# Optimization experiments

Hardware: AMD Instinct MI355X
Metric: run time of the kernel (lower is better)

Reference implementation:

```python
import jax, jax.numpy as jnp
import numpy as np
from jax import lax

B, S, D, H, HFF, T = 256, 33, 42, 128, 256, 20
BN_EPS = 1e-5

def _bn(x, g, b):
    # eval-mode BatchNorm1d with running_mean=0, running_var=1
    return x * (g / jnp.sqrt(1.0 + BN_EPS)) + b

def _gelu(x):
    return jax.nn.gelu(x, approximate=False)  # torch default GELU (exact)

def setup_inputs() -> dict:
    key = jax.random.key(0)
    ks = iter(jax.random.split(key, 48))
    w = lambda shp, s=0.02: jax.random.normal(next(ks), shp, dtype=jnp.float32) * s
    z = lambda shp: jnp.zeros(shp, jnp.float32)
    o = lambda shp: jnp.ones(shp, jnp.float32)
    inp = {
        'interaction_path': jax.random.normal(next(ks), (B, S, D), dtype=jnp.float32),
        'timestamps': jnp.broadcast_to(jnp.arange(S, dtype=jnp.float32) * 0.1, (B, S)),
        # initial encoder: Linear(42->128), BN, GELU, Linear(128->128), BN
        'enc_w1': w((D, H)), 'enc_b1': z(H), 'enc_g1': o(H), 'enc_be1': z(H),
        'enc_w2': w((H, H)), 'enc_b2': z(H), 'enc_g2': o(H), 'enc_be2': z(H),
        # vector field: 128->256 (BN,GELU), 256->256 (BN,GELU) x2, 256->5376
        'vf_w0': w((H, HFF)), 'vf_b0': z(HFF), 'vf_g0': o(HFF), 'vf_be0': z(HFF),
        'vf_w1': w((HFF, HFF)), 'vf_b1': z(HFF), 'vf_g1': o(HFF), 'vf_be1': z(HFF),
        'vf_w2': w((HFF, HFF)), 'vf_b2': z(HFF), 'vf_g2': o(HFF), 'vf_be2': z(HFF),
        'vf_w3': w((HFF, H * D)), 'vf_b3': z(H * D),
        # multihead attention (seq_len = 1 -> softmax is identically 1)
        'wv': w((H, H)), 'bv': z(H), 'wo': w((H, H)), 'bo': z(H),
        # 20 trait decoders, stacked: 128->64->32->1
        'dw1': w((T, H, 64)), 'db1': z((T, 64)),
        'dw2': w((T, 64, 32)), 'db2': z((T, 32)),
        'dw3': w((T, 32, 1)), 'db3': z((T, 1)),
    }
    return inp

def reference(interaction_path, timestamps,
              enc_w1, enc_b1, enc_g1, enc_be1, enc_w2, enc_b2, enc_g2, enc_be2,
              vf_w0, vf_b0, vf_g0, vf_be0, vf_w1, vf_b1, vf_g1, vf_be1,
              vf_w2, vf_b2, vf_g2, vf_be2, vf_w3, vf_b3,
              wv, bv, wo, bo,
              dw1, db1, dw2, db2, dw3, db3):
    b = interaction_path.shape[0]
    # ---- initial encoder on X[:, 0] ----
    x0 = interaction_path[:, 0]                      # [B, D]
    h = _gelu(_bn(x0 @ enc_w1 + enc_b1, enc_g1, enc_be1))
    z0 = _bn(h @ enc_w2 + enc_b2, enc_g2, enc_be2)   # [B, H]

    # ---- CDE vector field: z -> [B, H, D] ----
    def vf(zz):
        y = _gelu(_bn(zz @ vf_w0 + vf_b0, vf_g0, vf_be0))
        y = _gelu(_bn(y @ vf_w1 + vf_b1, vf_g1, vf_be1))
        y = _gelu(_bn(y @ vf_w2 + vf_b2, vf_g2, vf_be2))
        return (y @ vf_w3 + vf_b3).reshape(b, H, D)

    def g(zz, dxdt):  # f(z) @ dX/dt  -> [B, H]
        return jnp.einsum('bhd,bd->bh', vf(zz), dxdt)

    # linear-interpolation control path: piecewise-constant derivative
    t = timestamps[0]                                # [S]
    dt = t[1:] - t[:-1]                              # [S-1]
    dX = interaction_path[:, 1:] - interaction_path[:, :-1]   # [B, S-1, D]
    dXdt = dX / dt[None, :, None]                    # [B, S-1, D]

    def step(zz, x):
        dxdt, hstep = x
        k1 = g(zz, dxdt)
        k2 = g(zz + 0.5 * hstep * k1, dxdt)
        k3 = g(zz + 0.5 * hstep * k2, dxdt)
        k4 = g(zz + hstep * k3, dxdt)
        return zz + (hstep / 6.0) * (k1 + 2.0 * k2 + 2.0 * k3 + k4), None

    zT, _ = lax.scan(step, z0, (jnp.swapaxes(dXdt, 0, 1), dt))  # [B, H]

    # ---- self-attention over a length-1 sequence: softmax==1 -> out_proj(v) ----
    attended = (zT @ wv + bv) @ wo + bo              # [B, H]

    # ---- 20 trait decoders (stacked / vectorized) ----
    h1 = _gelu(jnp.einsum('bh,thd->tbd', attended, dw1) + db1[:, None, :])
    h2 = _gelu(jnp.einsum('tbd,tde->tbe', h1, dw2) + db2[:, None, :])
    out = jax.nn.sigmoid(jnp.einsum('tbe,teo->tbo', h2, dw3) + db3[:, None, :])
    return jnp.transpose(out[..., 0], (1, 0))        # [B, 20]
```

## Files before the change

### kernel.cpp

```cpp
#include <hip/hip_runtime.h>
#include <cstdint>

constexpr int B    = 256;
constexpr int S    = 33;
constexpr int D    = 42;
constexpr int H    = 128;
constexpr int HFF  = 256;
constexpr int T    = 20;
constexpr int NSTEP = S - 1;
constexpr int DP   = D / 2;
constexpr int ADW  = 8192;
constexpr int CH   = 16;
#define BN_SCALE 0.9999950000374997f

typedef _Float16 h2v __attribute__((ext_vector_type(2)));
union UH2 { uint32_t u; h2v h; };

__device__ __forceinline__ float fdot2u(uint32_t a, uint32_t b, float c) {
    UH2 x, y; x.u = a; y.u = b;
    return __builtin_amdgcn_fdot2(x.h, y.h, c, false);
}
__device__ __forceinline__ uint32_t packh2(float a, float b) {
    UH2 u; u.h = h2v{(_Float16)a, (_Float16)b}; return u.u;
}
__device__ __forceinline__ float gelu_exact(float x) {
    return 0.5f * x * (1.0f + erff(x * 0.70710678118654752f));
}
__device__ __forceinline__ float gelu_fast(float x) {
    float inner = x * (1.0f + 0.044715f * x * x);
    float E = __expf(1.5957691216f * inner);
    return x * E * __frcp_rn(E + 1.0f);
}

__global__ void pack_kernel(const float* __restrict__ w0, const float* __restrict__ w1,
                            const float* __restrict__ w2, const float* __restrict__ w3,
                            uint32_t* __restrict__ wcol, uint32_t* __restrict__ wq) {
    int idx = blockIdx.x * 256 + threadIdx.x;
    if (idx < 160 * 512) {
        int r = idx >> 9, t = idx & 511;
        int j = t >> 1, half = t & 1;
        float a, bb;
        if (r < 32)      { int ip = half * 32 + r;      a = w0[(2*ip)*HFF + j]; bb = w0[(2*ip+1)*HFF + j]; }
        else if (r < 96) { int ip = half * 64 + (r-32); a = w1[(2*ip)*HFF + j]; bb = w1[(2*ip+1)*HFF + j]; }
        else             { int ip = half * 64 + (r-96); a = w2[(2*ip)*HFF + j]; bb = w2[(2*ip+1)*HFF + j]; }
        wcol[idx] = packh2(a, bb);
    }
    if (idx < 8192 * 84) {
        int u = idx / 84, r = idx % 84;
        int k = u >> 7, h = u & 127;
        int row = r / 21, dp = r % 21;
        int e = 4 * k + row;
        wq[idx] = packh2(w3[e * (H * D) + h * D + 2 * dp],
                         w3[e * (H * D) + h * D + 2 * dp + 1]);
    }
}

__global__ void prep_kernel(const float* __restrict__ path, const float* __restrict__ ts,
                            const float* __restrict__ ew1, const float* __restrict__ eb1,
                            const float* __restrict__ eg1, const float* __restrict__ ebe1,
                            const float* __restrict__ ew2, const float* __restrict__ eb2,
                            const float* __restrict__ eg2, const float* __restrict__ ebe2,
                            const float* __restrict__ b3,
                            float* __restrict__ zbuf, uint32_t* __restrict__ dxdtp,
                            float* __restrict__ bd3g, float* __restrict__ dtb) {
    __shared__ float x0[D], hb[H], dxs[NSTEP][D];
    int b = blockIdx.x, tid = threadIdx.x;
    if (tid < D) x0[tid] = path[b * S * D + tid];
    __syncthreads();
    {
        float acc = eb1[tid];
        for (int d = 0; d < D; ++d) acc += x0[d] * ew1[d * H + tid];
        hb[tid] = gelu_exact(acc * (eg1[tid] * BN_SCALE) + ebe1[tid]);
    }
    __syncthreads();
    {
        float acc = eb2[tid];
        for (int i = 0; i < H; ++i) acc += hb[i] * ew2[i * H + tid];
        zbuf[b * H + tid] = acc * (eg2[tid] * BN_SCALE) + ebe2[tid];
    }
    for (int idx = tid; idx < NSTEP * DP; idx += 128) {
        int s = idx / DP, jj = idx % DP;
        float dtv = ts[s + 1] - ts[s];
        int base = b * S * D + s * D + 2 * jj;
        float v0 = (path[base + D] - path[base]) / dtv;
        float v1 = (path[base + D + 1] - path[base + 1]) / dtv;
        dxs[s][2 * jj] = v0; dxs[s][2 * jj + 1] = v1;
        dxdtp[(s * B + b) * DP + jj] = packh2(v0, v1);
    }
    __syncthreads();
    for (int s = 0; s < NSTEP; ++s) {
        float a = 0.f;
        for (int d = 0; d < D; ++d) a += b3[tid * D + d] * dxs[s][d];
        bd3g[(size_t)(s * B + b) * H + tid] = a;
    }
    if (b == 0 && tid < NSTEP) dtb[tid] = ts[tid + 1] - ts[tid];
}

__global__ void __launch_bounds__(256) aphase_kernel(
    const uint32_t* __restrict__ wq, const uint32_t* __restrict__ dxdtp,
    uint32_t* __restrict__ Ach, int s0) {
    __shared__ uint32_t dxs[128][24];
    int t = threadIdx.x;
    int ub = blockIdx.x & 63, sbc = blockIdx.x >> 6;
    int hu = ub * 256 + t;
    uint32_t wr[42];
    const uint32_t* wp = wq + (size_t)hu * 42;
#pragma unroll
    for (int r = 0; r < 42; ++r) wr[r] = wp[r];
    for (int idx = t; idx < 128 * DP; idx += 256) {
        int i = idx / DP, j2 = idx % DP;
        int sbl = sbc * 128 + i;
        int s = s0 + (sbl >> 8), b = sbl & 255;
        dxs[i][j2] = dxdtp[(size_t)(s * B + b) * DP + j2];
    }
    __syncthreads();
    unsigned short* As = (unsigned short*)Ach;
    for (int i = 0; i < 128; ++i) {
        int sbl = sbc * 128 + i;
        uint32_t dxr[21];
        {
            const uint32_t* row = dxs[i];
            *(uint4*)&dxr[0]  = *(const uint4*)&row[0];
            *(uint4*)&dxr[4]  = *(const uint4*)&row[4];
            *(uint4*)&dxr[8]  = *(const uint4*)&row[8];
            *(uint4*)&dxr[12] = *(const uint4*)&row[12];
            *(uint4*)&dxr[16] = *(const uint4*)&row[16];
            dxr[20] = row[20];
        }
        float a0 = 0.f, a1 = 0.f;
#pragma unroll
        for (int j = 0; j < 21; ++j) {
            a0 = fdot2u(wr[j],      dxr[j], a0);
            a1 = fdot2u(wr[21 + j], dxr[j], a1);
        }
        uint32_t P = packh2(a0, a1) + 0x00800080u;
        uint32_t Q = __builtin_amdgcn_perm(0u, P, 0x0C0C0301u);
        As[(size_t)sbl * (2 * ADW) + hu] = (unsigned short)Q;
    }
}

__global__ void __launch_bounds__(512, 1) scan_kernel(
    const uint32_t* __restrict__ wcol, const uint32_t* __restrict__ Ach,
    const float* __restrict__ vb0, const float* __restrict__ vg0, const float* __restrict__ vbe0,
    const float* __restrict__ vb1, const float* __restrict__ vg1, const float* __restrict__ vbe1,
    const float* __restrict__ vb2, const float* __restrict__ vg2, const float* __restrict__ vbe2,
    const float* __restrict__ bd3g, const float* __restrict__ dtb,
    float* __restrict__ zbuf, int s0) {
    __shared__ uint32_t ABUF[2][ADW];
    __shared__ uint32_t zzPd[72];
    __shared__ uint32_t yA[136], yB[136], yC[136];
    __shared__ float psum[4][128];
    int t = threadIdx.x, b = blockIdx.x;
    int j = t >> 1, half = t & 1;
    int h = t & 127, g = t >> 7;
    uint32_t w0h[32], w1h[64], w2h[64];
#pragma unroll
    for (int r = 0; r < 32; ++r) w0h[r] = wcol[r * 512 + t];
#pragma unroll
    for (int r = 0; r < 64; ++r) w1h[r] = wcol[(32 + r) * 512 + t];
#pragma unroll
    for (int r = 0; r < 64; ++r) w2h[r] = wcol[(96 + r) * 512 + t];
    float c0s = vg0[j] * BN_SCALE, c0o = vb0[j] * c0s + vbe0[j];
    float c1s = vg1[j] * BN_SCALE, c1o = vb1[j] * c1s + vbe1[j];
    float c2s = vg2[j] * BN_SCALE, c2o = vb2[j] * c2s + vbe2[j];
    float zf = zbuf[b * H + h];
    {
        const uint4* Ag = (const uint4*)(Ach + (size_t)b * ADW);
        uint4 a0 = Ag[t], a1 = Ag[512 + t], a2 = Ag[1024 + t], a3 = Ag[1536 + t];
        uint4* Ad = (uint4*)ABUF[0];
        Ad[t] = a0; Ad[512 + t] = a1; Ad[1024 + t] = a2; Ad[1536 + t] = a3;
    }
    if (t < 128) {
        float zhi = __shfl_down(zf, 1, 64);
        if ((t & 1) == 0) {
            int ip = t >> 1;
            zzPd[(ip >> 5) * 36 + (ip & 31)] = packh2(zf, zhi);
        }
    }
    __syncthreads();

    for (int sl = 0; sl < CH; ++sl) {
        int s = s0 + sl;
        float hstep = dtb[s];
        float bd3 = bd3g[(size_t)(s * B + b) * H + h];
        uint4 p0, p1, p2, p3;
        {
            int sn = (sl + 1 < CH) ? sl + 1 : sl;
            const uint4* Ag = (const uint4*)(Ach + (size_t)(sn * B + b) * ADW);
            p0 = Ag[t]; p1 = Ag[512 + t]; p2 = Ag[1024 + t]; p3 = Ag[1536 + t];
        }
        const uint32_t* AL = ABUF[sl & 1];
        float ksum = 0.f, kcur = 0.f;
        for (int r = 0; r < 4; ++r) {
            {
                float p = 0.f;
                const uint4* zq = (const uint4*)(zzPd + half * 36);
#pragma unroll
                for (int u4 = 0; u4 < 8; ++u4) {
                    uint4 zv = zq[u4];
                    p = fdot2u(w0h[4*u4+0], zv.x, p); p = fdot2u(w0h[4*u4+1], zv.y, p);
                    p = fdot2u(w0h[4*u4+2], zv.z, p); p = fdot2u(w0h[4*u4+3], zv.w, p);
                }
                p += __shfl_xor(p, 1, 64);
                float v = gelu_fast(p * c0s + c0o);
                float vhi = __shfl_down(v, 2, 64);
                if ((t & 3) == 0) {
                    int ip = t >> 2;
                    yA[(ip >> 6) * 68 + (ip & 63)] = packh2(v, vhi);
                }
            }
            __syncthreads();
            {
                float p = 0.f;
                const uint4* yq = (const uint4*)(yA + half * 68);
#pragma unroll
                for (int u4 = 0; u4 < 16; ++u4) {
                    uint4 yv = yq[u4];
                    p = fdot2u(w1h[4*u4+0], yv.x, p); p = fdot2u(w1h[4*u4+1], yv.y, p);
                    p = fdot2u(w1h[4*u4+2], yv.z, p); p = fdot2u(w1h[4*u4+3], yv.w, p);
                }
                p += __shfl_xor(p, 1, 64);
                float v = gelu_fast(p * c1s + c1o);
                float vhi = __shfl_down(v, 2, 64);
                if ((t & 3) == 0) {
                    int ip = t >> 2;
                    yB[(ip >> 6) * 68 + (ip & 63)] = packh2(v, vhi);
                }
            }
            __syncthreads();
            {
                float p = 0.f;
                const uint4* yq = (const uint4*)(yB + half * 68);
#pragma unroll
                for (int u4 = 0; u4 < 16; ++u4) {
                    uint4 yv = yq[u4];
                    p = fdot2u(w2h[4*u4+0], yv.x, p); p = fdot2u(w2h[4*u4+1], yv.y, p);
                    p = fdot2u(w2h[4*u4+2], yv.z, p); p = fdot2u(w2h[4*u4+3], yv.w, p);
                }
                p += __shfl_xor(p, 1, 64);
                float v = gelu_fast(p * c2s + c2o);
                float vhi = __shfl_down(v, 2, 64);
                if ((t & 3) == 0) {
                    int ip = t >> 2;
                    yC[(ip >> 6) * 68 + (ip & 63)] = packh2(v, vhi);
                }
            }
            __syncthreads();
            {
                float p = 0.f, p2 = 0.f;
                int ybase = (g >> 1) * 68 + (g & 1) * 32;
                const uint4* yq = (const uint4*)(yC + ybase);
#pragma unroll
                for (int kk = 0; kk < 8; ++kk) {
                    uint4 yv = yq[kk];
                    int k0 = g * 16 + 2 * kk;
                    uint32_t Qa = AL[k0 * 128 + h];
                    uint32_t Qb = AL[(k0 + 1) * 128 + h];
                    p  = fdot2u(__builtin_amdgcn_perm(0u, Qa, 0x010C000Cu), yv.x, p);
                    p2 = fdot2u(__builtin_amdgcn_perm(0u, Qa, 0x030C020Cu), yv.y, p2);
                    p  = fdot2u(__builtin_amdgcn_perm(0u, Qb, 0x010C000Cu), yv.z, p);
                    p2 = fdot2u(__builtin_amdgcn_perm(0u, Qb, 0x030C020Cu), yv.w, p2);
                }
                psum[g][h] = p + p2;
            }
            __syncthreads();
            if (t < 128) {
                kcur = bd3 + psum[0][h] + psum[1][h] + psum[2][h] + psum[3][h];
                float wsm = (r == 1 || r == 2) ? 2.f : 1.f;
                ksum += wsm * kcur;
                float zz;
                if (r < 3) {
                    float cin = (r == 2) ? 1.f : 0.5f;
                    zz = zf + cin * hstep * kcur;
                } else {
                    zf += hstep * (1.f / 6.f) * ksum;
                    zz = zf;
                }
                float zhi = __shfl_down(zz, 1, 64);
                if ((t & 1) == 0) {
                    int ip = t >> 1;
                    zzPd[(ip >> 5) * 36 + (ip & 31)] = packh2(zz, zhi);
                }
            }
            if (r == 3) {
                uint4* Ad = (uint4*)ABUF[(sl + 1) & 1];
                Ad[t] = p0; Ad[512 + t] = p1; Ad[1024 + t] = p2; Ad[1536 + t] = p3;
            }
            __syncthreads();
        }
    }
    if (t < 128) zbuf[b * H + h] = zf;
}

__global__ void att_kernel(const float* __restrict__ zbuf,
                           const float* __restrict__ wv, const float* __restrict__ bv,
                           const float* __restrict__ wo, const float* __restrict__ bo,
                           float* __restrict__ att) {
    __shared__ float zl[H], v[H];
    int b = blockIdx.x, tid = threadIdx.x;
    zl[tid] = zbuf[b * H + tid];
    __syncthreads();
    {
        float acc = bv[tid];
#pragma unroll 8
        for (int i = 0; i < H; ++i) acc += zl[i] * wv[i * H + tid];
        v[tid] = acc;
    }
    __syncthreads();
    {
        float acc = bo[tid];
#pragma unroll 8
        for (int i = 0; i < H; ++i) acc += v[i] * wo[i * H + tid];
        att[b * H + tid] = acc;
    }
}

__global__ void __launch_bounds__(64) dec_kernel(
    const float* __restrict__ att,
    const float* __restrict__ dw1, const float* __restrict__ db1,
    const float* __restrict__ dw2, const float* __restrict__ db2,
    const float* __restrict__ dw3, const float* __restrict__ db3,
    float* __restrict__ out) {
    int bid = blockIdx.x;
    int t = bid >> 8, b = bid & 255;
    int tid = threadIdx.x;
    __shared__ float al[H], h1l[64];
    al[tid] = att[b * H + tid];
    al[tid + 64] = att[b * H + tid + 64];
    __syncthreads();
    {
        float acc = db1[t * 64 + tid];
#pragma unroll 8
        for (int i = 0; i < H; ++i) acc += al[i] * dw1[t * H * 64 + i * 64 + tid];
        h1l[tid] = gelu_exact(acc);
    }
    __syncthreads();
    float v = 0.f;
    if (tid < 32) {
        float acc = db2[t * 32 + tid];
#pragma unroll 8
        for (int i = 0; i < 64; ++i) acc += h1l[i] * dw2[t * 64 * 32 + i * 32 + tid];
        v = gelu_exact(acc) * dw3[t * 32 + tid];
    }
#pragma unroll
    for (int off = 16; off >= 1; off >>= 1) v += __shfl_down(v, off, 64);
    if (tid == 0) out[b * T + t] = 1.f / (1.f + expf(-(v + db3[t])));
}

extern "C" void kernel_launch(void* const* d_in, const int* in_sizes, int n_in,
                              void* d_out, int out_size, void* d_ws, size_t ws_size,
                              hipStream_t stream) {
    const float* path = (const float*)d_in[0];
    const float* ts   = (const float*)d_in[1];
    const float* ew1  = (const float*)d_in[2];
    const float* eb1  = (const float*)d_in[3];
    const float* eg1  = (const float*)d_in[4];
    const float* ebe1 = (const float*)d_in[5];
    const float* ew2  = (const float*)d_in[6];
    const float* eb2  = (const float*)d_in[7];
    const float* eg2  = (const float*)d_in[8];
    const float* ebe2 = (const float*)d_in[9];
    const float* vw0  = (const float*)d_in[10];
    const float* vb0  = (const float*)d_in[11];
    const float* vg0  = (const float*)d_in[12];
    const float* vbe0 = (const float*)d_in[13];
    const float* vw1  = (const float*)d_in[14];
    const float* vb1  = (const float*)d_in[15];
    const float* vg1  = (const float*)d_in[16];
    const float* vbe1 = (const float*)d_in[17];
    const float* vw2  = (const float*)d_in[18];
    const float* vb2  = (const float*)d_in[19];
    const float* vg2  = (const float*)d_in[20];
    const float* vbe2 = (const float*)d_in[21];
    const float* vw3  = (const float*)d_in[22];
    const float* vb3  = (const float*)d_in[23];
    const float* wv   = (const float*)d_in[24];
    const float* bv   = (const float*)d_in[25];
    const float* wo   = (const float*)d_in[26];
    const float* bo   = (const float*)d_in[27];
    const float* dw1  = (const float*)d_in[28];
    const float* db1  = (const float*)d_in[29];
    const float* dw2  = (const float*)d_in[30];
    const float* db2  = (const float*)d_in[31];
    const float* dw3  = (const float*)d_in[32];
    const float* db3  = (const float*)d_in[33];

    char* ws = (char*)d_ws;
    size_t off = 0;
    auto take = [&](size_t bytes) { char* p = ws + off; off += (bytes + 255) & ~(size_t)255; return p; };
    uint32_t* Ach   = (uint32_t*)take((size_t)CH * B * ADW * 4);
    uint32_t* dxdtp = (uint32_t*)take((size_t)NSTEP * B * DP * 4);
    float*    bd3g  = (float*)take((size_t)NSTEP * B * H * 4);
    float*    dtb   = (float*)take(NSTEP * 4);
    float*    zbuf  = (float*)take((size_t)B * H * 4);
    float*    att   = (float*)take((size_t)B * H * 4);
    uint32_t* wcol  = (uint32_t*)take((size_t)160 * 512 * 4);
    uint32_t* wq    = (uint32_t*)take((size_t)8192 * 84 * 4);

    pack_kernel<<<(8192 * 84 + 255) / 256, 256, 0, stream>>>(vw0, vw1, vw2, vw3, wcol, wq);
    prep_kernel<<<B, 128, 0, stream>>>(path, ts, ew1, eb1, eg1, ebe1,
                                       ew2, eb2, eg2, ebe2, vb3, zbuf, dxdtp, bd3g, dtb);
    for (int c = 0; c < NSTEP / CH; ++c) {
        aphase_kernel<<<2048, 256, 0, stream>>>(wq, dxdtp, Ach, c * CH);
        scan_kernel<<<B, 512, 0, stream>>>(wcol, Ach,
                                           vb0, vg0, vbe0, vb1, vg1, vbe1, vb2, vg2, vbe2,
                                           bd3g, dtb, zbuf, c * CH);
    }
    att_kernel<<<B, 128, 0, stream>>>(zbuf, wv, bv, wo, bo, att);
    dec_kernel<<<T * B, 64, 0, stream>>>(att, dw1, db1, dw2, db2, dw3, db3, (float*)d_out);
}
```

Baseline: 662.6 us.

## Store scan MLP weights as 8-bit e5 floats and split dot accumulators

The three hidden-layer weight matrices of the vector-field MLP are packed as 8-bit e5m2-style values (fp16 high bytes) instead of fp16. This halves the register footprint of the per-thread weight arrays in the scan kernel, at the cost of perm instructions to expand each weight back to fp16 before every dot2. The aphase kernel drops its shared-memory staging of dxdt and reads it directly from global memory. Both kernels split their dot-product chains into two independent accumulators to shorten dependency chains. Weight precision drops to roughly 2 mantissa bits, which risks accuracy.

```diff
diff --git a/kernel.cpp b/kernel.cpp
--- a/kernel.cpp
+++ b/kernel.cpp
@@ -23,6 +23,11 @@
 __device__ __forceinline__ uint32_t packh2(float a, float b) {
     UH2 u; u.h = h2v{(_Float16)a, (_Float16)b}; return u.u;
 }
+__device__ __forceinline__ uint32_t pack4e5(float a, float b, float c, float d) {
+    uint32_t P01 = packh2(a, b) + 0x00800080u;
+    uint32_t P23 = packh2(c, d) + 0x00800080u;
+    return __builtin_amdgcn_perm(P23, P01, 0x07050301u);
+}
 __device__ __forceinline__ float gelu_exact(float x) {
     return 0.5f * x * (1.0f + erff(x * 0.70710678118654752f));
 }
@@ -34,16 +39,17 @@
 
 __global__ void pack_kernel(const float* __restrict__ w0, const float* __restrict__ w1,
                             const float* __restrict__ w2, const float* __restrict__ w3,
-                            uint32_t* __restrict__ wcol, uint32_t* __restrict__ wq) {
+                            uint32_t* __restrict__ wcol8, uint32_t* __restrict__ wq) {
     int idx = blockIdx.x * 256 + threadIdx.x;
-    if (idx < 160 * 512) {
+    if (idx < 80 * 512) {
         int r = idx >> 9, t = idx & 511;
         int j = t >> 1, half = t & 1;
-        float a, bb;
-        if (r < 32)      { int ip = half * 32 + r;      a = w0[(2*ip)*HFF + j]; bb = w0[(2*ip+1)*HFF + j]; }
-        else if (r < 96) { int ip = half * 64 + (r-32); a = w1[(2*ip)*HFF + j]; bb = w1[(2*ip+1)*HFF + j]; }
-        else             { int ip = half * 64 + (r-96); a = w2[(2*ip)*HFF + j]; bb = w2[(2*ip+1)*HFF + j]; }
-        wcol[idx] = packh2(a, bb);
+        const float* w; int p0;
+        if (r < 16)      { w = w0; p0 = half * 32 + 2 * r; }
+        else if (r < 48) { w = w1; p0 = half * 64 + 2 * (r - 16); }
+        else             { w = w2; p0 = half * 64 + 2 * (r - 48); }
+        wcol8[idx] = pack4e5(w[(2 * p0) * HFF + j],     w[(2 * p0 + 1) * HFF + j],
+                             w[(2 * p0 + 2) * HFF + j], w[(2 * p0 + 3) * HFF + j]);
     }
     if (idx < 8192 * 84) {
         int u = idx / 84, r = idx % 84;
@@ -99,7 +105,6 @@
 __global__ void __launch_bounds__(256) aphase_kernel(
     const uint32_t* __restrict__ wq, const uint32_t* __restrict__ dxdtp,
     uint32_t* __restrict__ Ach, int s0) {
-    __shared__ uint32_t dxs[128][24];
     int t = threadIdx.x;
     int ub = blockIdx.x & 63, sbc = blockIdx.x >> 6;
     int hu = ub * 256 + t;
@@ -107,40 +112,28 @@
     const uint32_t* wp = wq + (size_t)hu * 42;
 #pragma unroll
     for (int r = 0; r < 42; ++r) wr[r] = wp[r];
-    for (int idx = t; idx < 128 * DP; idx += 256) {
-        int i = idx / DP, j2 = idx % DP;
-        int sbl = sbc * 128 + i;
-        int s = s0 + (sbl >> 8), b = sbl & 255;
-        dxs[i][j2] = dxdtp[(size_t)(s * B + b) * DP + j2];
-    }
-    __syncthreads();
     unsigned short* As = (unsigned short*)Ach;
     for (int i = 0; i < 128; ++i) {
         int sbl = sbc * 128 + i;
+        int s = s0 + (sbl >> 8), b = sbl & 255;
+        const uint32_t* dxp = dxdtp + (size_t)(s * B + b) * DP;
         uint32_t dxr[21];
-        {
-            const uint32_t* row = dxs[i];
-            *(uint4*)&dxr[0]  = *(const uint4*)&row[0];
-            *(uint4*)&dxr[4]  = *(const uint4*)&row[4];
-            *(uint4*)&dxr[8]  = *(const uint4*)&row[8];
-            *(uint4*)&dxr[12] = *(const uint4*)&row[12];
-            *(uint4*)&dxr[16] = *(const uint4*)&row[16];
-            dxr[20] = row[20];
+#pragma unroll
+        for (int j = 0; j < 21; ++j) dxr[j] = dxp[j];
+        float a0x = 0.f, a0y = 0.f, a1x = 0.f, a1y = 0.f;
+#pragma unroll
+        for (int j = 0; j < 21; ++j) {
+            if (j & 1) { a0y = fdot2u(wr[j], dxr[j], a0y); a1y = fdot2u(wr[21 + j], dxr[j], a1y); }
+            else       { a0x = fdot2u(wr[j], dxr[j], a0x); a1x = fdot2u(wr[21 + j], dxr[j], a1x); }
         }
-        float a0 = 0.f, a1 = 0.f;
-#pragma unroll
-        for (int j = 0; j < 21; ++j) {
-            a0 = fdot2u(wr[j],      dxr[j], a0);
-            a1 = fdot2u(wr[21 + j], dxr[j], a1);
-        }
-        uint32_t P = packh2(a0, a1) + 0x00800080u;
+        uint32_t P = packh2(a0x + a0y, a1x + a1y) + 0x00800080u;
         uint32_t Q = __builtin_amdgcn_perm(0u, P, 0x0C0C0301u);
         As[(size_t)sbl * (2 * ADW) + hu] = (unsigned short)Q;
     }
 }
 
 __global__ void __launch_bounds__(512, 1) scan_kernel(
-    const uint32_t* __restrict__ wcol, const uint32_t* __restrict__ Ach,
+    const uint32_t* __restrict__ wcol8, const uint32_t* __restrict__ Ach,
     const float* __restrict__ vb0, const float* __restrict__ vg0, const float* __restrict__ vbe0,
     const float* __restrict__ vb1, const float* __restrict__ vg1, const float* __restrict__ vbe1,
     const float* __restrict__ vb2, const float* __restrict__ vg2, const float* __restrict__ vbe2,
@@ -153,13 +146,13 @@
     int t = threadIdx.x, b = blockIdx.x;
     int j = t >> 1, half = t & 1;
     int h = t & 127, g = t >> 7;
-    uint32_t w0h[32], w1h[64], w2h[64];
-#pragma unroll
-    for (int r = 0; r < 32; ++r) w0h[r] = wcol[r * 512 + t];
-#pragma unroll
-    for (int r = 0; r < 64; ++r) w1h[r] = wcol[(32 + r) * 512 + t];
-#pragma unroll
-    for (int r = 0; r < 64; ++r) w2h[r] = wcol[(96 + r) * 512 + t];
+    uint32_t w0q[16], w1q[32], w2q[32];
+#pragma unroll
+    for (int r = 0; r < 16; ++r) w0q[r] = wcol8[r * 512 + t];
+#pragma unroll
+    for (int r = 0; r < 32; ++r) w1q[r] = wcol8[(16 + r) * 512 + t];
+#pragma unroll
+    for (int r = 0; r < 32; ++r) w2q[r] = wcol8[(48 + r) * 512 + t];
     float c0s = vg0[j] * BN_SCALE, c0o = vb0[j] * c0s + vbe0[j];
     float c1s = vg1[j] * BN_SCALE, c1o = vb1[j] * c1s + vbe1[j];
     float c2s = vg2[j] * BN_SCALE, c2o = vb2[j] * c2s + vbe2[j];
@@ -193,14 +186,18 @@
         float ksum = 0.f, kcur = 0.f;
         for (int r = 0; r < 4; ++r) {
             {
-                float p = 0.f;
+                float pA = 0.f, pB = 0.f;
                 const uint4* zq = (const uint4*)(zzPd + half * 36);
 #pragma unroll
                 for (int u4 = 0; u4 < 8; ++u4) {
                     uint4 zv = zq[u4];
-                    p = fdot2u(w0h[4*u4+0], zv.x, p); p = fdot2u(w0h[4*u4+1], zv.y, p);
-                    p = fdot2u(w0h[4*u4+2], zv.z, p); p = fdot2u(w0h[4*u4+3], zv.w, p);
-                }
+                    uint32_t Wa = w0q[2 * u4], Wb = w0q[2 * u4 + 1];
+                    pA = fdot2u(__builtin_amdgcn_perm(0u, Wa, 0x010C000Cu), zv.x, pA);
+                    pA = fdot2u(__builtin_amdgcn_perm(0u, Wa, 0x030C020Cu), zv.y, pA);
+                    pB = fdot2u(__builtin_amdgcn_perm(0u, Wb, 0x010C000Cu), zv.z, pB);
+                    pB = fdot2u(__builtin_amdgcn_perm(0u, Wb, 0x030C020Cu), zv.w, pB);
+                }
+                float p = pA + pB;
                 p += __shfl_xor(p, 1, 64);
                 float v = gelu_fast(p * c0s + c0o);
                 float vhi = __shfl_down(v, 2, 64);
@@ -211,14 +208,18 @@
             }
             __syncthreads();
             {
-                float p = 0.f;
+                float pA = 0.f, pB = 0.f;
                 const uint4* yq = (const uint4*)(yA + half * 68);
 #pragma unroll
                 for (int u4 = 0; u4 < 16; ++u4) {
                     uint4 yv = yq[u4];
-                    p = fdot2u(w1h[4*u4+0], yv.x, p); p = fdot2u(w1h[4*u4+1], yv.y, p);
-                    p = fdot2u(w1h[4*u4+2], yv.z, p); p = fdot2u(w1h[4*u4+3], yv.w, p);
-                }
+                    uint32_t Wa = w1q[2 * u4], Wb = w1q[2 * u4 + 1];
+                    pA = fdot2u(__builtin_amdgcn_perm(0u, Wa, 0x010C000Cu), yv.x, pA);
+                    pA = fdot2u(__builtin_amdgcn_perm(0u, Wa, 0x030C020Cu), yv.y, pA);
+                    pB = fdot2u(__builtin_amdgcn_perm(0u, Wb, 0x010C000Cu), yv.z, pB);
+                    pB = fdot2u(__builtin_amdgcn_perm(0u, Wb, 0x030C020Cu), yv.w, pB);
+                }
+                float p = pA + pB;
                 p += __shfl_xor(p, 1, 64);
                 float v = gelu_fast(p * c1s + c1o);
                 float vhi = __shfl_down(v, 2, 64);
@@ -229,14 +230,18 @@
             }
             __syncthreads();
             {
-                float p = 0.f;
+                float pA = 0.f, pB = 0.f;
                 const uint4* yq = (const uint4*)(yB + half * 68);
 #pragma unroll
                 for (int u4 = 0; u4 < 16; ++u4) {
                     uint4 yv = yq[u4];
-                    p = fdot2u(w2h[4*u4+0], yv.x, p); p = fdot2u(w2h[4*u4+1], yv.y, p);
-                    p = fdot2u(w2h[4*u4+2], yv.z, p); p = fdot2u(w2h[4*u4+3], yv.w, p);
-                }
+                    uint32_t Wa = w2q[2 * u4], Wb = w2q[2 * u4 + 1];
+                    pA = fdot2u(__builtin_amdgcn_perm(0u, Wa, 0x010C000Cu), yv.x, pA);
+                    pA = fdot2u(__builtin_amdgcn_perm(0u, Wa, 0x030C020Cu), yv.y, pA);
+                    pB = fdot2u(__builtin_amdgcn_perm(0u, Wb, 0x010C000Cu), yv.z, pB);
+                    pB = fdot2u(__builtin_amdgcn_perm(0u, Wb, 0x030C020Cu), yv.w, pB);
+                }
+                float p = pA + pB;
                 p += __shfl_xor(p, 1, 64);
                 float v = gelu_fast(p * c2s + c2o);
                 float vhi = __shfl_down(v, 2, 64);
@@ -394,15 +399,15 @@
     float*    dtb   = (float*)take(NSTEP * 4);
     float*    zbuf  = (float*)take((size_t)B * H * 4);
     float*    att   = (float*)take((size_t)B * H * 4);
-    uint32_t* wcol  = (uint32_t*)take((size_t)160 * 512 * 4);
+    uint32_t* wcol8 = (uint32_t*)take((size_t)80 * 512 * 4);
     uint32_t* wq    = (uint32_t*)take((size_t)8192 * 84 * 4);
 
-    pack_kernel<<<(8192 * 84 + 255) / 256, 256, 0, stream>>>(vw0, vw1, vw2, vw3, wcol, wq);
+    pack_kernel<<<(8192 * 84 + 255) / 256, 256, 0, stream>>>(vw0, vw1, vw2, vw3, wcol8, wq);
     prep_kernel<<<B, 128, 0, stream>>>(path, ts, ew1, eb1, eg1, ebe1,
                                        ew2, eb2, eg2, ebe2, vb3, zbuf, dxdtp, bd3g, dtb);
     for (int c = 0; c < NSTEP / CH; ++c) {
         aphase_kernel<<<2048, 256, 0, stream>>>(wq, dxdtp, Ach, c * CH);
-        scan_kernel<<<B, 512, 0, stream>>>(wcol, Ach,
+        scan_kernel<<<B, 512, 0, stream>>>(wcol8, Ach,
                                            vb0, vg0, vbe0, vb1, vg1, vbe1, vb2, vg2, vbe2,
                                            bd3g, dtb, zbuf, c * CH);
     }
```

Result: slower. 689.7 us (+4.1%).
